# Kernel tuning notes

Measured on AMD Instinct MI355X. Metric: run time of the kernel, lower is better.

Reference implementation:

```python
import jax, jax.numpy as jnp
import numpy as np

N = 50000          # nodes
E = 1600000        # edges
H = 8              # heads
F = 16             # out feats per head (np1class)
IN = 256           # in feats
NEG_SLOPE = 0.2    # DGL GATConv default leaky_relu slope


def setup_inputs() -> dict:
    key = jax.random.key(0)
    ks = jax.random.split(key, 7)
    x = jax.random.normal(ks[0], (N, IN), dtype=jnp.float32)
    W = jax.random.normal(ks[1], (IN, H * F), dtype=jnp.float32) * 0.05
    attn_l = jax.random.normal(ks[2], (H, F), dtype=jnp.float32) * 0.05
    attn_r = jax.random.normal(ks[3], (H, F), dtype=jnp.float32) * 0.05
    bias = jax.random.normal(ks[4], (H * F,), dtype=jnp.float32) * 0.05
    src = jax.random.randint(ks[5], (E,), 0, N, dtype=jnp.int64)
    dst = jax.random.randint(ks[6], (E,), 0, N, dtype=jnp.int64)
    return {"x": x, "W": W, "attn_l": attn_l, "attn_r": attn_r,
            "bias": bias, "src": src, "dst": dst}


def reference(x, W, attn_l, attn_r, bias, src, dst):
    # Linear projection to heads: [N, H, F]
    feat = (x @ W).reshape(N, H, F)
    # Per-node attention halves: [N, H]
    el = jnp.einsum('nhf,hf->nh', feat, attn_l)
    er = jnp.einsum('nhf,hf->nh', feat, attn_r)
    # Edge scores: e = leaky_relu(el[src] + er[dst])  -> [E, H]
    e = jax.nn.leaky_relu(el[src] + er[dst], negative_slope=NEG_SLOPE)
    # Segment softmax over incoming edges of each destination node
    m = jax.ops.segment_max(e, dst, num_segments=N)           # [N, H]
    m = jnp.where(jnp.isfinite(m), m, 0.0)                    # empty segments
    m = jax.lax.stop_gradient(m)
    ex = jnp.exp(e - m[dst])                                  # [E, H]
    s = jax.ops.segment_sum(ex, dst, num_segments=N)          # [N, H]
    a = ex / jnp.maximum(s[dst], 1e-9)                        # [E, H]
    # Weighted aggregation of source features: [N, H, F]
    msg = a[:, :, None] * feat[src]
    rst = jax.ops.segment_sum(msg, dst, num_segments=N)
    rst = rst + bias.reshape(H, F)
    # Classifier: mean over heads -> [N, F]
    return rst.mean(axis=1)
```

## Files before the change

### kernel.cpp

```cpp
#include <hip/hip_runtime.h>
#include <hip/hip_bf16.h>

#define NH 8
#define NF 16
#define NIN 256
#define HF 128
#define CAP 3072
#define BCH 4096

typedef __attribute__((ext_vector_type(8))) short bf16x8;
typedef __attribute__((ext_vector_type(4))) float f32x4;

__device__ __forceinline__ unsigned short f2bf(float f) {
    union { float f; unsigned int u; } v; v.f = f;
    unsigned int r = v.u + 0x7FFFu + ((v.u >> 16) & 1u);
    return (unsigned short)(r >> 16);
}
__device__ __forceinline__ float bf2f(unsigned short b) {
    union { unsigned int u; float f; } v; v.u = ((unsigned int)b) << 16;
    return v.f;
}

#define GROWS 128
__global__ __launch_bounds__(256) void gemm_mfma(const float* __restrict__ A,
                                                 const float* __restrict__ W,
                                                 const float* __restrict__ attn_l,
                                                 const float* __restrict__ attn_r,
                                                 unsigned short* __restrict__ featb,
                                                 float* __restrict__ el,
                                                 float* __restrict__ er, int M) {
    __shared__ unsigned short AsH[32][264];
    __shared__ unsigned short AsL[32][264];
    const int tid = threadIdx.x;
    const int wave = tid >> 6, lane = tid & 63;
    const int quad = lane >> 4, lq = lane & 15;
    const int row0 = blockIdx.x * GROWS;

    bf16x8 bfrag[8][2];
#pragma unroll
    for (int h2 = 0; h2 < 2; h2++) {
        const int col = (wave * 2 + h2) * 16 + lq;
#pragma unroll
        for (int kk = 0; kk < 8; kk++) {
            const int kb = kk * 32 + quad * 8;
            bf16x8 f;
#pragma unroll
            for (int j = 0; j < 8; j++)
                f[j] = (short)f2bf(W[(size_t)(kb + j) * HF + col]);
            bfrag[kk][h2] = f;
        }
    }
    const float al0 = attn_l[(wave * 2 + 0) * 16 + lq];
    const float al1 = attn_l[(wave * 2 + 1) * 16 + lq];
    const float ar0 = attn_r[(wave * 2 + 0) * 16 + lq];
    const float ar1 = attn_r[(wave * 2 + 1) * 16 + lq];

    const int srow = tid >> 3;

    for (int c = 0; c < 4; c++) {
        const int crow0 = row0 + c * 32;
        __syncthreads();
#pragma unroll
        for (int i = 0; i < 8; i++) {
            const int col = ((tid & 7) + i * 8) * 4;
            const int gr = crow0 + srow;
            float4 v = make_float4(0.f, 0.f, 0.f, 0.f);
            if (gr < M) v = *(const float4*)&A[(size_t)gr * NIN + col];
            const unsigned short h0 = f2bf(v.x), h1 = f2bf(v.y),
                                 h2b = f2bf(v.z), h3 = f2bf(v.w);
            *(ushort4*)&AsH[srow][col] = make_ushort4(h0, h1, h2b, h3);
            *(ushort4*)&AsL[srow][col] =
                make_ushort4(f2bf(v.x - bf2f(h0)), f2bf(v.y - bf2f(h1)),
                             f2bf(v.z - bf2f(h2b)), f2bf(v.w - bf2f(h3)));
        }
        __syncthreads();
#pragma unroll
        for (int s = 0; s < 2; s++) {
            f32x4 acc0 = {0.f, 0.f, 0.f, 0.f};
            f32x4 acc1 = {0.f, 0.f, 0.f, 0.f};
            const int ar = s * 16 + lq;
#pragma unroll
            for (int kk = 0; kk < 8; kk++) {
                const bf16x8 ah = *(const bf16x8*)&AsH[ar][kk * 32 + quad * 8];
                const bf16x8 al = *(const bf16x8*)&AsL[ar][kk * 32 + quad * 8];
                acc0 = __builtin_amdgcn_mfma_f32_16x16x32_bf16(ah, bfrag[kk][0], acc0, 0, 0, 0);
                acc1 = __builtin_amdgcn_mfma_f32_16x16x32_bf16(ah, bfrag[kk][1], acc1, 0, 0, 0);
                acc0 = __builtin_amdgcn_mfma_f32_16x16x32_bf16(al, bfrag[kk][0], acc0, 0, 0, 0);
                acc1 = __builtin_amdgcn_mfma_f32_16x16x32_bf16(al, bfrag[kk][1], acc1, 0, 0, 0);
            }
#pragma unroll
            for (int r = 0; r < 4; r++) {
                const int gr = crow0 + s * 16 + quad * 4 + r;
                float pl0 = acc0[r] * al0, pr0 = acc0[r] * ar0;
                float pl1 = acc1[r] * al1, pr1 = acc1[r] * ar1;
#pragma unroll
                for (int m = 1; m < 16; m <<= 1) {
                    pl0 += __shfl_xor(pl0, m, 64);
                    pr0 += __shfl_xor(pr0, m, 64);
                    pl1 += __shfl_xor(pl1, m, 64);
                    pr1 += __shfl_xor(pr1, m, 64);
                }
                if (gr < M) {
                    featb[(size_t)gr * HF + (wave * 2 + 0) * 16 + lq] = f2bf(acc0[r]);
                    featb[(size_t)gr * HF + (wave * 2 + 1) * 16 + lq] = f2bf(acc1[r]);
                    if (lq == 0) {
                        el[(size_t)gr * NH + wave * 2 + 0] = pl0;
                        el[(size_t)gr * NH + wave * 2 + 1] = pl1;
                        er[(size_t)gr * NH + wave * 2 + 0] = pr0;
                        er[(size_t)gr * NH + wave * 2 + 1] = pr1;
                    }
                }
            }
        }
    }
}

__global__ __launch_bounds__(256) void bin_kernel(const int* __restrict__ src,
                                                  const int* __restrict__ dst,
                                                  unsigned int* __restrict__ binned,
                                                  unsigned int* __restrict__ runtab,
                                                  int E, int NB) {
    __shared__ unsigned int hist[784];
    __shared__ unsigned int offs[784];
    __shared__ unsigned short lpos[BCH];
    __shared__ unsigned int obuf[BCH];
    __shared__ int dcache[BCH];
    __shared__ unsigned int wsum[4];
    __shared__ unsigned int sbase;
    const int blk = blockIdx.x, t = threadIdx.x;
    const int base = blk * BCH;
    const int cnt = min(BCH, E - base);
    const int lane = t & 63, w = t >> 6;
    for (int b = t; b < NB; b += 256) hist[b] = 0;
    for (int i = t; i < cnt; i += 256) dcache[i] = dst[base + i];
    if (t == 0) sbase = 0;
    __syncthreads();
    for (int i = t; i < cnt; i += 256)
        lpos[i] = (unsigned short)atomicAdd(&hist[dcache[i] >> 6], 1u);
    __syncthreads();
    for (int c0 = 0; c0 < NB; c0 += 256) {
        const int idx = c0 + t;
        const unsigned int v = (idx < NB) ? hist[idx] : 0;
        unsigned int incl = v;
#pragma unroll
        for (int off = 1; off < 64; off <<= 1) {
            const unsigned int x = __shfl_up(incl, off, 64);
            if (lane >= off) incl += x;
        }
        if (lane == 63) wsum[w] = incl;
        __syncthreads();
        unsigned int wbase = 0;
        for (int k = 0; k < w; k++) wbase += wsum[k];
        const unsigned int tot = wsum[0] + wsum[1] + wsum[2] + wsum[3];
        const unsigned int excl = sbase + wbase + incl - v;
        if (idx < NB) {
            offs[idx] = excl;
            runtab[(size_t)blk * NB + idx] = excl | (v << 16);
        }
        __syncthreads();
        if (t == 0) sbase += tot;
        __syncthreads();
    }
    for (int i = t; i < cnt; i += 256) {
        const int d = dcache[i];
        obuf[offs[d >> 6] + lpos[i]] =
            (unsigned int)src[base + i] | ((unsigned int)(d & 63) << 16);
    }
    __syncthreads();
    for (int i = t; i < cnt; i += 256) binned[(size_t)base + i] = obuf[i];
}

__global__ __launch_bounds__(256) void csr_kernel(const unsigned int* __restrict__ binned,
                                                  const unsigned int* __restrict__ runtab,
                                                  int* __restrict__ nodeinfo,
                                                  unsigned short* __restrict__ srcsw,
                                                  int N, int NB, int nbb) {
    __shared__ unsigned int eary[CAP];
    __shared__ unsigned short sSrc[CAP];
    __shared__ unsigned short roff[512];
    __shared__ unsigned short rcntl[512];
    __shared__ int rbase[512];
    __shared__ int len[64], cur[64];
    __shared__ unsigned int wsum[4];
    __shared__ unsigned int sbase;
    const int b = blockIdx.x, t = threadIdx.x;
    const int node0 = b << 6;
    const int lane = t & 63, w = t >> 6;
    if (t == 0) sbase = 0;
    __syncthreads();
    for (int c0 = 0; c0 < nbb; c0 += 256) {
        const int r = c0 + t;
        const unsigned int e = (r < nbb) ? runtab[(size_t)r * NB + b] : 0;
        const unsigned int v = e >> 16;
        unsigned int incl = v;
#pragma unroll
        for (int off = 1; off < 64; off <<= 1) {
            const unsigned int x = __shfl_up(incl, off, 64);
            if (lane >= off) incl += x;
        }
        if (lane == 63) wsum[w] = incl;
        __syncthreads();
        unsigned int wbase = 0;
        for (int k = 0; k < w; k++) wbase += wsum[k];
        const unsigned int tot = wsum[0] + wsum[1] + wsum[2] + wsum[3];
        if (r < nbb) {
            roff[r] = (unsigned short)(e & 0xFFFFu);
            rcntl[r] = (unsigned short)v;
            rbase[r] = (int)(sbase + wbase + incl - v);
        }
        __syncthreads();
        if (t == 0) sbase += tot;
        __syncthreads();
    }
    const int tot = (int)sbase;
    for (int r = t; r < nbb; r += 256) {
        const int off = (int)roff[r];
        const int pb = rbase[r];
        const int rc = (int)rcntl[r];
        const unsigned int* bp = &binned[(size_t)r * BCH + off];
        for (int j = 0; j < rc; j++) eary[pb + j] = bp[j];
    }
    if (t < 64) len[t] = 0;
    __syncthreads();
    for (int i = t; i < tot; i += 256) atomicAdd(&len[eary[i] >> 16], 1);
    __syncthreads();
    if (t < 64) {
        const int v = len[t];
        int incl = v;
#pragma unroll
        for (int off = 1; off < 64; off <<= 1) {
            const int x = __shfl_up(incl, off, 64);
            if (t >= off) incl += x;
        }
        const int excl = incl - v;
        cur[t] = excl;
        if (node0 + t < N) nodeinfo[node0 + t] = excl | (v << 16);
    }
    __syncthreads();
    for (int i = t; i < tot; i += 256) {
        const unsigned int p = eary[i];
        const int pos = atomicAdd(&cur[p >> 16], 1);
        sSrc[pos] = (unsigned short)(p & 0xFFFFu);
    }
    __syncthreads();
    unsigned short* sw = &srcsw[(size_t)b * CAP];
    for (int i = t; i < tot; i += 256) sw[i] = sSrc[i];
}

#define WIN 64
__global__ __launch_bounds__(256) void agg_kernel(const int* __restrict__ nodeinfo,
                                                  const unsigned short* __restrict__ srcsw,
                                                  const float* __restrict__ el,
                                                  const float* __restrict__ er,
                                                  const unsigned short* __restrict__ featb,
                                                  const float* __restrict__ bias,
                                                  float* __restrict__ out, int N) {
    __shared__ float lds_sc[4][WIN][8];
    __shared__ int lds_src[4][WIN];
    const int tid = threadIdx.x;
    const int w = tid >> 6, lane = tid & 63;
    const int n = blockIdx.x * 4 + w;
    if (n >= N) return;

    const int info = nodeinfo[n];
    const int begin = (n >> 6) * CAP + (info & 0xFFFF);
    const int end = begin + (info >> 16);
    const int hA = lane & 7, eA = lane >> 3;
    const float er_h = er[(size_t)n * NH + hA];
    const int hB = lane >> 3, fB2 = lane & 7;

    float2 acc = make_float2(0.f, 0.f);
    float psum = 0.f;
    for (int base = begin; base < end; base += WIN) {
        const int cn = min(WIN, end - base);
        __builtin_amdgcn_wave_barrier();
#pragma unroll
        for (int rep = 0; rep < 8; rep++) {
            const int ei = rep * 8 + eA;
            if (ei < cn) {
                const int si = (int)srcsw[base + ei];
                if (hA == 0) lds_src[w][ei] = si;
                float v = el[(size_t)si * NH + hA] + er_h;
                v = v > 0.f ? v : 0.2f * v;
                const float sc = __expf(v);
                lds_sc[w][ei][hA] = sc;
                psum += sc;
            }
        }
        __builtin_amdgcn_wave_barrier();
        for (int b0 = 0; b0 < cn; b0 += 16) {
            unsigned int fv[16];
#pragma unroll
            for (int j = 0; j < 16; j++) {
                const int ej = b0 + j;
                const int sj = lds_src[w][ej];
                fv[j] = (ej < cn)
                            ? *(const unsigned int*)&featb[(size_t)sj * HF + hB * 16 + fB2 * 2]
                            : 0u;
            }
#pragma unroll
            for (int j = 0; j < 16; j++) {
                const int ej = b0 + j;
                const float sc = (ej < cn) ? lds_sc[w][ej][hB] : 0.f;
                acc.x = fmaf(sc, bf2f((unsigned short)(fv[j] & 0xFFFFu)), acc.x);
                acc.y = fmaf(sc, bf2f((unsigned short)(fv[j] >> 16)), acc.y);
            }
        }
    }

    float s = psum;
    s += __shfl_xor(s, 8, 64);
    s += __shfl_xor(s, 16, 64);
    s += __shfl_xor(s, 32, 64);
    const float s_h = __shfl(s, hB, 64);
    const float inv = 1.f / fmaxf(s_h, 1e-9f);
    float2 val;
    val.x = acc.x * inv + bias[hB * 16 + fB2 * 2];
    val.y = acc.y * inv + bias[hB * 16 + fB2 * 2 + 1];
    val.x += __shfl_xor(val.x, 8, 64);
    val.x += __shfl_xor(val.x, 16, 64);
    val.x += __shfl_xor(val.x, 32, 64);
    val.y += __shfl_xor(val.y, 8, 64);
    val.y += __shfl_xor(val.y, 16, 64);
    val.y += __shfl_xor(val.y, 32, 64);
    if (lane < 8) {
        float2 o;
        o.x = val.x * 0.125f;
        o.y = val.y * 0.125f;
        *(float2*)&out[(size_t)n * 16 + lane * 2] = o;
    }
}

extern "C" void kernel_launch(void* const* d_in, const int* in_sizes, int n_in,
                              void* d_out, int out_size, void* d_ws, size_t ws_size,
                              hipStream_t stream) {
    const float* x      = (const float*)d_in[0];
    const float* W      = (const float*)d_in[1];
    const float* attn_l = (const float*)d_in[2];
    const float* attn_r = (const float*)d_in[3];
    const float* bias   = (const float*)d_in[4];
    const int*   src    = (const int*)d_in[5];
    const int*   dst    = (const int*)d_in[6];
    float* out = (float*)d_out;

    const int N = in_sizes[0] / NIN;
    const int E = in_sizes[5];
    const int NB = (N + 63) >> 6;
    const int nbb = (E + BCH - 1) / BCH;

    char* w = (char*)d_ws;
    unsigned short* featb = (unsigned short*)w; w += (size_t)N * HF * 2;
    float* el     = (float*)w; w += (size_t)N * NH * 4;
    float* er     = (float*)w; w += (size_t)N * NH * 4;
    int* nodeinfo = (int*)w;   w += (size_t)N * 4;
    unsigned int* binned = (unsigned int*)w; w += (size_t)nbb * BCH * 4;
    unsigned int* runtab = (unsigned int*)w; w += (size_t)nbb * NB * 4;
    unsigned short* srcsw = (unsigned short*)w;

    gemm_mfma<<<(N + GROWS - 1) / GROWS, 256, 0, stream>>>(x, W, attn_l, attn_r,
                                                           featb, el, er, N);
    bin_kernel<<<nbb, 256, 0, stream>>>(src, dst, binned, runtab, E, NB);
    csr_kernel<<<NB, 256, 0, stream>>>(binned, runtab, nodeinfo, srcsw, N, NB, nbb);
    agg_kernel<<<(N + 3) / 4, 256, 0, stream>>>(nodeinfo, srcsw, el, er, featb, bias,
                                                out, N);
}
```

Measured before the change: 228.6 us.

## Merge GEMM and edge binning into one launch; make aggregation grid-stride

The independent GEMM projection and edge-binning kernels now run as one launch, with block index choosing the role and a shared LDS pool sized for the larger of the two. This removes one launch and lets the two independent stages overlap on the GPU. The aggregation kernel also switches from one wave per node to a fixed grid of 2048 blocks, each wave looping over nodes. The merged kernel's LDS footprint is the binning size for every block, which may lower occupancy for the GEMM blocks, and the fixed grid may balance load less evenly.

```diff
diff --git a/kernel.cpp b/kernel.cpp
--- a/kernel.cpp
+++ b/kernel.cpp
@@ -21,20 +21,35 @@
     return v.f;
 }
 
+struct GemmLds {
+    unsigned short AsH[32][264];
+    unsigned short AsL[32][264];
+};
+struct BinLds {
+    unsigned int hist[784];
+    unsigned int offs[784];
+    unsigned short lpos[BCH];
+    unsigned int obuf[BCH];
+    int dcache[BCH];
+    unsigned int wsum[4];
+    unsigned int sbase;
+};
+#define POOLSZ ((sizeof(BinLds) > sizeof(GemmLds)) ? sizeof(BinLds) : sizeof(GemmLds))
+
 #define GROWS 128
-__global__ __launch_bounds__(256) void gemm_mfma(const float* __restrict__ A,
-                                                 const float* __restrict__ W,
-                                                 const float* __restrict__ attn_l,
-                                                 const float* __restrict__ attn_r,
-                                                 unsigned short* __restrict__ featb,
-                                                 float* __restrict__ el,
-                                                 float* __restrict__ er, int M) {
-    __shared__ unsigned short AsH[32][264];
-    __shared__ unsigned short AsL[32][264];
+__device__ __forceinline__ void gemm_body(char* pool, int bid,
+                                          const float* __restrict__ A,
+                                          const float* __restrict__ W,
+                                          const float* __restrict__ attn_l,
+                                          const float* __restrict__ attn_r,
+                                          unsigned short* __restrict__ featb,
+                                          float* __restrict__ el,
+                                          float* __restrict__ er, int M) {
+    GemmLds& gl = *reinterpret_cast<GemmLds*>(pool);
     const int tid = threadIdx.x;
     const int wave = tid >> 6, lane = tid & 63;
     const int quad = lane >> 4, lq = lane & 15;
-    const int row0 = blockIdx.x * GROWS;
+    const int row0 = bid * GROWS;
 
     bf16x8 bfrag[8][2];
 #pragma unroll
@@ -68,8 +83,8 @@
             if (gr < M) v = *(const float4*)&A[(size_t)gr * NIN + col];
             const unsigned short h0 = f2bf(v.x), h1 = f2bf(v.y),
                                  h2b = f2bf(v.z), h3 = f2bf(v.w);
-            *(ushort4*)&AsH[srow][col] = make_ushort4(h0, h1, h2b, h3);
-            *(ushort4*)&AsL[srow][col] =
+            *(ushort4*)&gl.AsH[srow][col] = make_ushort4(h0, h1, h2b, h3);
+            *(ushort4*)&gl.AsL[srow][col] =
                 make_ushort4(f2bf(v.x - bf2f(h0)), f2bf(v.y - bf2f(h1)),
                              f2bf(v.z - bf2f(h2b)), f2bf(v.w - bf2f(h3)));
         }
@@ -81,8 +96,8 @@
             const int ar = s * 16 + lq;
 #pragma unroll
             for (int kk = 0; kk < 8; kk++) {
-                const bf16x8 ah = *(const bf16x8*)&AsH[ar][kk * 32 + quad * 8];
-                const bf16x8 al = *(const bf16x8*)&AsL[ar][kk * 32 + quad * 8];
+                const bf16x8 ah = *(const bf16x8*)&gl.AsH[ar][kk * 32 + quad * 8];
+                const bf16x8 al = *(const bf16x8*)&gl.AsL[ar][kk * 32 + quad * 8];
                 acc0 = __builtin_amdgcn_mfma_f32_16x16x32_bf16(ah, bfrag[kk][0], acc0, 0, 0, 0);
                 acc1 = __builtin_amdgcn_mfma_f32_16x16x32_bf16(ah, bfrag[kk][1], acc1, 0, 0, 0);
                 acc0 = __builtin_amdgcn_mfma_f32_16x16x32_bf16(al, bfrag[kk][0], acc0, 0, 0, 0);
@@ -115,59 +130,73 @@
     }
 }
 
-__global__ __launch_bounds__(256) void bin_kernel(const int* __restrict__ src,
-                                                  const int* __restrict__ dst,
-                                                  unsigned int* __restrict__ binned,
-                                                  unsigned int* __restrict__ runtab,
-                                                  int E, int NB) {
-    __shared__ unsigned int hist[784];
-    __shared__ unsigned int offs[784];
-    __shared__ unsigned short lpos[BCH];
-    __shared__ unsigned int obuf[BCH];
-    __shared__ int dcache[BCH];
-    __shared__ unsigned int wsum[4];
-    __shared__ unsigned int sbase;
-    const int blk = blockIdx.x, t = threadIdx.x;
+__device__ __forceinline__ void bin_body(char* pool, int blk,
+                                         const int* __restrict__ src,
+                                         const int* __restrict__ dst,
+                                         unsigned int* __restrict__ binned,
+                                         unsigned int* __restrict__ runtab,
+                                         int E, int NB) {
+    BinLds& bl = *reinterpret_cast<BinLds*>(pool);
+    const int t = threadIdx.x;
     const int base = blk * BCH;
     const int cnt = min(BCH, E - base);
     const int lane = t & 63, w = t >> 6;
-    for (int b = t; b < NB; b += 256) hist[b] = 0;
-    for (int i = t; i < cnt; i += 256) dcache[i] = dst[base + i];
-    if (t == 0) sbase = 0;
+    for (int b = t; b < NB; b += 256) bl.hist[b] = 0;
+    for (int i = t; i < cnt; i += 256) bl.dcache[i] = dst[base + i];
+    if (t == 0) bl.sbase = 0;
     __syncthreads();
     for (int i = t; i < cnt; i += 256)
-        lpos[i] = (unsigned short)atomicAdd(&hist[dcache[i] >> 6], 1u);
+        bl.lpos[i] = (unsigned short)atomicAdd(&bl.hist[bl.dcache[i] >> 6], 1u);
     __syncthreads();
     for (int c0 = 0; c0 < NB; c0 += 256) {
         const int idx = c0 + t;
-        const unsigned int v = (idx < NB) ? hist[idx] : 0;
+        const unsigned int v = (idx < NB) ? bl.hist[idx] : 0;
         unsigned int incl = v;
 #pragma unroll
         for (int off = 1; off < 64; off <<= 1) {
             const unsigned int x = __shfl_up(incl, off, 64);
             if (lane >= off) incl += x;
         }
-        if (lane == 63) wsum[w] = incl;
+        if (lane == 63) bl.wsum[w] = incl;
         __syncthreads();
         unsigned int wbase = 0;
-        for (int k = 0; k < w; k++) wbase += wsum[k];
-        const unsigned int tot = wsum[0] + wsum[1] + wsum[2] + wsum[3];
-        const unsigned int excl = sbase + wbase + incl - v;
+        for (int k = 0; k < w; k++) wbase += bl.wsum[k];
+        const unsigned int tot = bl.wsum[0] + bl.wsum[1] + bl.wsum[2] + bl.wsum[3];
+        const unsigned int excl = bl.sbase + wbase + incl - v;
         if (idx < NB) {
-            offs[idx] = excl;
+            bl.offs[idx] = excl;
             runtab[(size_t)blk * NB + idx] = excl | (v << 16);
         }
         __syncthreads();
-        if (t == 0) sbase += tot;
+        if (t == 0) bl.sbase += tot;
         __syncthreads();
     }
     for (int i = t; i < cnt; i += 256) {
-        const int d = dcache[i];
-        obuf[offs[d >> 6] + lpos[i]] =
+        const int d = bl.dcache[i];
+        bl.obuf[bl.offs[d >> 6] + bl.lpos[i]] =
             (unsigned int)src[base + i] | ((unsigned int)(d & 63) << 16);
     }
     __syncthreads();
-    for (int i = t; i < cnt; i += 256) binned[(size_t)base + i] = obuf[i];
+    for (int i = t; i < cnt; i += 256) binned[(size_t)base + i] = bl.obuf[i];
+}
+
+__global__ __launch_bounds__(256) void gemm_bin(const float* __restrict__ A,
+                                                const float* __restrict__ W,
+                                                const float* __restrict__ attn_l,
+                                                const float* __restrict__ attn_r,
+                                                unsigned short* __restrict__ featb,
+                                                float* __restrict__ el,
+                                                float* __restrict__ er, int M,
+                                                const int* __restrict__ src,
+                                                const int* __restrict__ dst,
+                                                unsigned int* __restrict__ binned,
+                                                unsigned int* __restrict__ runtab,
+                                                int E, int NB, int GB) {
+    __shared__ __align__(16) char pool[POOLSZ];
+    if ((int)blockIdx.x < GB)
+        gemm_body(pool, blockIdx.x, A, W, attn_l, attn_r, featb, el, er, M);
+    else
+        bin_body(pool, blockIdx.x - GB, src, dst, binned, runtab, E, NB);
 }
 
 __global__ __launch_bounds__(256) void csr_kernel(const unsigned int* __restrict__ binned,
@@ -248,6 +277,7 @@
 }
 
 #define WIN 64
+#define AGGB 2048
 __global__ __launch_bounds__(256) void agg_kernel(const int* __restrict__ nodeinfo,
                                                   const unsigned short* __restrict__ srcsw,
                                                   const float* __restrict__ el,
@@ -259,75 +289,77 @@
     __shared__ int lds_src[4][WIN];
     const int tid = threadIdx.x;
     const int w = tid >> 6, lane = tid & 63;
-    const int n = blockIdx.x * 4 + w;
-    if (n >= N) return;
-
-    const int info = nodeinfo[n];
-    const int begin = (n >> 6) * CAP + (info & 0xFFFF);
-    const int end = begin + (info >> 16);
     const int hA = lane & 7, eA = lane >> 3;
-    const float er_h = er[(size_t)n * NH + hA];
     const int hB = lane >> 3, fB2 = lane & 7;
-
-    float2 acc = make_float2(0.f, 0.f);
-    float psum = 0.f;
-    for (int base = begin; base < end; base += WIN) {
-        const int cn = min(WIN, end - base);
-        __builtin_amdgcn_wave_barrier();
-#pragma unroll
-        for (int rep = 0; rep < 8; rep++) {
-            const int ei = rep * 8 + eA;
-            if (ei < cn) {
-                const int si = (int)srcsw[base + ei];
-                if (hA == 0) lds_src[w][ei] = si;
-                float v = el[(size_t)si * NH + hA] + er_h;
-                v = v > 0.f ? v : 0.2f * v;
-                const float sc = __expf(v);
-                lds_sc[w][ei][hA] = sc;
-                psum += sc;
+    const int wgid = blockIdx.x * 4 + w;
+    const int nwaves = gridDim.x * 4;
+
+    for (int n = wgid; n < N; n += nwaves) {
+        const int info = nodeinfo[n];
+        const int begin = (n >> 6) * CAP + (info & 0xFFFF);
+        const int end = begin + (info >> 16);
+        const float er_h = er[(size_t)n * NH + hA];
+
+        float2 acc = make_float2(0.f, 0.f);
+        float psum = 0.f;
+        for (int base = begin; base < end; base += WIN) {
+            const int cn = min(WIN, end - base);
+            __builtin_amdgcn_wave_barrier();
+#pragma unroll
+            for (int rep = 0; rep < 8; rep++) {
+                const int ei = rep * 8 + eA;
+                if (ei < cn) {
+                    const int si = (int)srcsw[base + ei];
+                    if (hA == 0) lds_src[w][ei] = si;
+                    float v = el[(size_t)si * NH + hA] + er_h;
+                    v = v > 0.f ? v : 0.2f * v;
+                    const float sc = __expf(v);
+                    lds_sc[w][ei][hA] = sc;
+                    psum += sc;
+                }
             }
-        }
-        __builtin_amdgcn_wave_barrier();
-        for (int b0 = 0; b0 < cn; b0 += 16) {
-            unsigned int fv[16];
-#pragma unroll
-            for (int j = 0; j < 16; j++) {
-                const int ej = b0 + j;
-                const int sj = lds_src[w][ej];
-                fv[j] = (ej < cn)
-                            ? *(const unsigned int*)&featb[(size_t)sj * HF + hB * 16 + fB2 * 2]
-                            : 0u;
+            __builtin_amdgcn_wave_barrier();
+            for (int b0 = 0; b0 < cn; b0 += 16) {
+                unsigned int fv[16];
+#pragma unroll
+                for (int j = 0; j < 16; j++) {
+                    const int ej = b0 + j;
+                    const int sj = lds_src[w][ej];
+                    fv[j] = (ej < cn)
+                                ? *(const unsigned int*)&featb[(size_t)sj * HF + hB * 16 + fB2 * 2]
+                                : 0u;
+                }
+#pragma unroll
+                for (int j = 0; j < 16; j++) {
+                    const int ej = b0 + j;
+                    const float sc = (ej < cn) ? lds_sc[w][ej][hB] : 0.f;
+                    acc.x = fmaf(sc, bf2f((unsigned short)(fv[j] & 0xFFFFu)), acc.x);
+                    acc.y = fmaf(sc, bf2f((unsigned short)(fv[j] >> 16)), acc.y);
+                }
             }
-#pragma unroll
-            for (int j = 0; j < 16; j++) {
-                const int ej = b0 + j;
-                const float sc = (ej < cn) ? lds_sc[w][ej][hB] : 0.f;
-                acc.x = fmaf(sc, bf2f((unsigned short)(fv[j] & 0xFFFFu)), acc.x);
-                acc.y = fmaf(sc, bf2f((unsigned short)(fv[j] >> 16)), acc.y);
-            }
-        }
-    }
-
-    float s = psum;
-    s += __shfl_xor(s, 8, 64);
-    s += __shfl_xor(s, 16, 64);
-    s += __shfl_xor(s, 32, 64);
-    const float s_h = __shfl(s, hB, 64);
-    const float inv = 1.f / fmaxf(s_h, 1e-9f);
-    float2 val;
-    val.x = acc.x * inv + bias[hB * 16 + fB2 * 2];
-    val.y = acc.y * inv + bias[hB * 16 + fB2 * 2 + 1];
-    val.x += __shfl_xor(val.x, 8, 64);
-    val.x += __shfl_xor(val.x, 16, 64);
-    val.x += __shfl_xor(val.x, 32, 64);
-    val.y += __shfl_xor(val.y, 8, 64);
-    val.y += __shfl_xor(val.y, 16, 64);
-    val.y += __shfl_xor(val.y, 32, 64);
-    if (lane < 8) {
-        float2 o;
-        o.x = val.x * 0.125f;
-        o.y = val.y * 0.125f;
-        *(float2*)&out[(size_t)n * 16 + lane * 2] = o;
+        }
+
+        float s = psum;
+        s += __shfl_xor(s, 8, 64);
+        s += __shfl_xor(s, 16, 64);
+        s += __shfl_xor(s, 32, 64);
+        const float s_h = __shfl(s, hB, 64);
+        const float inv = 1.f / fmaxf(s_h, 1e-9f);
+        float2 val;
+        val.x = acc.x * inv + bias[hB * 16 + fB2 * 2];
+        val.y = acc.y * inv + bias[hB * 16 + fB2 * 2 + 1];
+        val.x += __shfl_xor(val.x, 8, 64);
+        val.x += __shfl_xor(val.x, 16, 64);
+        val.x += __shfl_xor(val.x, 32, 64);
+        val.y += __shfl_xor(val.y, 8, 64);
+        val.y += __shfl_xor(val.y, 16, 64);
+        val.y += __shfl_xor(val.y, 32, 64);
+        if (lane < 8) {
+            float2 o;
+            o.x = val.x * 0.125f;
+            o.y = val.y * 0.125f;
+            *(float2*)&out[(size_t)n * 16 + lane * 2] = o;
+        }
     }
 }
 
@@ -347,6 +379,7 @@
     const int E = in_sizes[5];
     const int NB = (N + 63) >> 6;
     const int nbb = (E + BCH - 1) / BCH;
+    const int GB = (N + GROWS - 1) / GROWS;
 
     char* w = (char*)d_ws;
     unsigned short* featb = (unsigned short*)w; w += (size_t)N * HF * 2;
@@ -357,10 +390,8 @@
     unsigned int* runtab = (unsigned int*)w; w += (size_t)nbb * NB * 4;
     unsigned short* srcsw = (unsigned short*)w;
 
-    gemm_mfma<<<(N + GROWS - 1) / GROWS, 256, 0, stream>>>(x, W, attn_l, attn_r,
-                                                           featb, el, er, N);
-    bin_kernel<<<nbb, 256, 0, stream>>>(src, dst, binned, runtab, E, NB);
+    gemm_bin<<<GB + nbb, 256, 0, stream>>>(x, W, attn_l, attn_r, featb, el, er, N,
+                                           src, dst, binned, runtab, E, NB, GB);
     csr_kernel<<<NB, 256, 0, stream>>>(binned, runtab, nodeinfo, srcsw, N, NB, nbb);
-    agg_kernel<<<(N + 3) / 4, 256, 0, stream>>>(nodeinfo, srcsw, el, er, featb, bias,
-                                                out, N);
-}
+    agg_kernel<<<AGGB, 256, 0, stream>>>(nodeinfo, srcsw, el, er, featb, bias, out, N);
+}
```

Measured after the change: 242.7 us. +6.2%, slower.
